# Performance work log

Measured on AMD Instinct MI355X. Metric: run time of the kernel, lower is better.

Reference implementation:

```python
import jax, jax.numpy as jnp
import numpy as np
from jax import lax

EPS = 1e-5
N_CROPS = 501
CROP_W = 500
RF = 65          # temporal receptive field
KS = 15          # conv1 kernel size
POOL = 3


def _bn(x, g, b, m, v, axis=1):
    shp = [1] * x.ndim
    shp[axis] = -1
    inv = g.reshape(shp) / jnp.sqrt(v.reshape(shp) + EPS)
    return (x - m.reshape(shp)) * inv + b.reshape(shp)


def setup_inputs() -> dict:
    key = jax.random.key(0)
    ks = jax.random.split(key, 16)
    B, C_IN, CH, T = 16, 1, 22, 1001
    F = 36
    OUT = 4
    FLAT = F * 43  # 1548 (corrected fc in_features; repo constant 504 is inconsistent)
    d = {
        "x": jax.random.normal(ks[0], (B, C_IN, CH, T), jnp.float32),
        # temporal conv [1,65]
        "w_t": jax.random.normal(ks[1], (F, 1, 1, RF), jnp.float32) * 0.1,
        "b_t": jax.random.normal(ks[2], (F,), jnp.float32) * 0.1,
        "bn_t_g": jax.random.uniform(ks[3], (F,), jnp.float32, 0.5, 1.5),
        "bn_t_b": jax.random.normal(ks[4], (F,), jnp.float32) * 0.1,
        "bn_t_m": jax.random.normal(ks[5], (F,), jnp.float32) * 0.1,
        "bn_t_v": jax.random.uniform(ks[6], (F,), jnp.float32, 0.5, 1.5),
        # spatial conv [22,1]
        "w_s": jax.random.normal(ks[7], (F, F, CH, 1), jnp.float32) * 0.05,
        "b_s": jax.random.normal(ks[8], (F,), jnp.float32) * 0.1,
        "bn_s_g": jax.random.uniform(ks[9], (F,), jnp.float32, 0.5, 1.5),
        "bn_s_b": jax.random.normal(ks[10], (F,), jnp.float32) * 0.1,
        "bn_s_m": jax.random.normal(ks[11], (F,), jnp.float32) * 0.1,
        "bn_s_v": jax.random.uniform(ks[12], (F,), jnp.float32, 0.5, 1.5),
        # conv1 [1,15] (as 1-D conv over time)
        "w_c": jax.random.normal(ks[13], (F, F, KS), jnp.float32) * 0.05,
        "b_c": jax.random.normal(ks[14], (F,), jnp.float32) * 0.1,
        "bn_c_g": jnp.ones((F,), jnp.float32),
        "bn_c_b": jnp.zeros((F,), jnp.float32),
        "bn_c_m": jnp.zeros((F,), jnp.float32),
        "bn_c_v": jnp.ones((F,), jnp.float32),
        # fc
        "w_fc": jax.random.normal(ks[15], (OUT, FLAT), jnp.float32) * 0.02,
        "b_fc": jnp.zeros((OUT,), jnp.float32),
    }
    return d


def reference(x, w_t, b_t, bn_t_g, bn_t_b, bn_t_m, bn_t_v,
              w_s, b_s, bn_s_g, bn_s_b, bn_s_m, bn_s_v,
              w_c, b_c, bn_c_g, bn_c_b, bn_c_m, bn_c_v,
              w_fc, b_fc):
    B = x.shape[0]
    F = w_t.shape[0]
    OUT = b_fc.shape[0]

    # temporal + spatial conv/BN/ELU are shift-invariant -> compute once over full T
    h = lax.conv_general_dilated(x, w_t, (1, 1), 'VALID',
                                 dimension_numbers=('NCHW', 'OIHW', 'NCHW'))
    h = h + b_t[None, :, None, None]                       # [B,36,22,937]
    h = jax.nn.elu(_bn(h, bn_t_g, bn_t_b, bn_t_m, bn_t_v))
    h = lax.conv_general_dilated(h, w_s, (1, 1), 'VALID',
                                 dimension_numbers=('NCHW', 'OIHW', 'NCHW'))
    h = h + b_s[None, :, None, None]                       # [B,36,1,937]
    h = jax.nn.elu(_bn(h, bn_s_g, bn_s_b, bn_s_m, bn_s_v))
    h = h[:, :, 0, :]                                      # [B,36,937]

    TW = CROP_W - RF + 1  # 436: temporal width of each crop after temporal conv

    def crop_logits(i):
        sl = lax.dynamic_slice_in_dim(h, i, TW, axis=2)    # [B,36,436]
        p1 = sl[:, :, :435].reshape(B, F, 145, POOL).mean(-1)  # avgpool1 -> [B,36,145]
        c = lax.conv_general_dilated(p1, w_c, (1,), 'VALID',
                                     dimension_numbers=('NCH', 'OIH', 'NCH'))
        c = c + b_c[None, :, None]                          # [B,36,131]
        c = jax.nn.elu(_bn(c, bn_c_g, bn_c_b, bn_c_m, bn_c_v))
        p2 = c[:, :, :129].reshape(B, F, 43, POOL).mean(-1)  # avgpool2 -> [B,36,43]
        flat = p2.reshape(B, -1)                            # [B,1548]
        return flat @ w_fc.T + b_fc                         # [B,OUT]

    def step(acc, i):
        return acc + crop_logits(i), None

    init = jnp.zeros((B, OUT), x.dtype)
    total, _ = lax.scan(step, init, jnp.arange(N_CROPS))
    return total / N_CROPS
```

## Files before the change

### kernel.cpp

```cpp
#include <hip/hip_runtime.h>

#define EPS 1e-5f
#define B 16
#define CH 22
#define CH2 24
#define T_IN 1001
#define F 36
#define RF 65
#define T1 937
#define FC 792
#define UN 885
#define PSP 944
#define KS 15
#define GN 295
#define WN 129
#define M43 43
#define BF 576
#define FLAT 1548

#define H2_OFF  0
#define A_OFF   539712
#define P_OFF   1049472
#define WTT_OFF 4617792
#define WST_OFF 4620132
#define WCQ_OFF 4651236
#define BN_OFF  4677156

__device__ __forceinline__ float elu_f(float v) {
    return v > 0.f ? v : (__expf(v) - 1.f);
}

__global__ __launch_bounds__(256) void k_prep(
    const float* __restrict__ w_t, const float* __restrict__ w_s,
    const float* __restrict__ w_c,
    const float* __restrict__ b_t, const float* __restrict__ g_t,
    const float* __restrict__ be_t,const float* __restrict__ m_t,
    const float* __restrict__ v_t,
    const float* __restrict__ b_s, const float* __restrict__ g_s,
    const float* __restrict__ be_s,const float* __restrict__ m_s,
    const float* __restrict__ v_s,
    const float* __restrict__ b_c, const float* __restrict__ g_c,
    const float* __restrict__ be_c,const float* __restrict__ m_c,
    const float* __restrict__ v_c, const float* __restrict__ b_fc,
    float* __restrict__ wtT, float* __restrict__ wsTp,
    float* __restrict__ wcQ, float* __restrict__ bnz,
    float* __restrict__ out)
{
    int i = blockIdx.x * 256 + threadIdx.x;
    if (i < F * RF)     { int k = i / F,  fi = i % F; wtT[i] = w_t[fi * RF + k]; }
    if (i < F * CH2 * F) {
        int fi = i / (CH2 * F);
        int r  = i % (CH2 * F);
        int ch = r / F, fo = r % F;
        wsTp[i] = (ch < CH) ? w_s[(fo * F + fi) * CH + ch] : 0.f;
    }
    if (i < 12 * 36 * 15 * 4) {
        int t3 = i / (36 * 15 * 4);
        int r  = i % (36 * 15 * 4);
        int f  = r / 60;
        int r2 = r % 60;
        int k  = r2 / 4, j = r2 % 4;
        wcQ[i] = (j < 3) ? w_c[((3 * t3 + j) * F + f) * KS + k] : 0.f;
    }
    if (i < F) {
        float s1 = g_t[i] * rsqrtf(v_t[i] + EPS);
        bnz[i]          = s1;
        bnz[F + i]      = (b_t[i] - m_t[i]) * s1 + be_t[i];
        float s2 = g_s[i] * rsqrtf(v_s[i] + EPS);
        bnz[2 * F + i]  = s2;
        bnz[3 * F + i]  = (b_s[i] - m_s[i]) * s2 + be_s[i];
        float s3 = g_c[i] * rsqrtf(v_c[i] + EPS);
        bnz[4 * F + i]  = s3;
        bnz[5 * F + i]  = (b_c[i] - m_c[i]) * s3 + be_c[i];
    }
    if (i < B * 4) out[i] = b_fc[i & 3];
}

__global__ __launch_bounds__(1024, 4) void k_fused(
    const float* __restrict__ x, const float* __restrict__ wtT,
    const float* __restrict__ wsTp, const float* __restrict__ bnz,
    float* __restrict__ h2)
{
    __shared__ float xs[CH2 * 128];
    __shared__ float comb[8][64][F];
    const int tid  = threadIdx.x;
    const int lane = tid & 63;
    const int w = __builtin_amdgcn_readfirstlane(tid >> 6);
    const int q = w >> 2;
    const int g = w & 3;
    const int b  = blockIdx.y;
    const int t0 = blockIdx.x * 64;

    for (int i = tid; i < CH2 * 128; i += 1024) {
        int ch = i >> 7, j = i & 127;
        int t = t0 + j; if (t > T_IN - 1) t = T_IN - 1;
        xs[i] = (ch < CH) ? x[(b * CH + ch) * T_IN + t] : 0.f;
    }
    __syncthreads();

    const int ch0 = q * 6;
    const int fi0 = g * 9;

    float acc[F];
    #pragma unroll
    for (int fo = 0; fo < F; ++fo) acc[fo] = 0.f;

    for (int c = 0; c < 6; ++c) {
        const float* xr = xs + (ch0 + c) * 128 + lane;

        float h1a[9];
        #pragma unroll
        for (int j = 0; j < 9; ++j) h1a[j] = 0.f;

        #pragma unroll 8
        for (int kp = 0; kp < 32; ++kp) {
            const int k = 2 * kp;
            float xv0 = xr[k];
            float xv1 = xr[k + 1];
            const float* w0 = wtT + k * F + fi0;
            const float* w1 = w0 + F;
            #pragma unroll
            for (int j = 0; j < 9; ++j) {
                h1a[j] += xv0 * w0[j];
                h1a[j] += xv1 * w1[j];
            }
        }
        {
            float xv = xr[64];
            const float* w64 = wtT + 64 * F + fi0;
            #pragma unroll
            for (int j = 0; j < 9; ++j) h1a[j] += xv * w64[j];
        }

        #pragma unroll
        for (int j = 0; j < 9; ++j)
            h1a[j] = elu_f(h1a[j] * bnz[fi0 + j] + bnz[F + fi0 + j]);

        #pragma unroll
        for (int j = 0; j < 9; ++j) {
            const float* wr = wsTp + ((fi0 + j) * CH2 + ch0 + c) * F;
            float e = h1a[j];
            #pragma unroll
            for (int fo = 0; fo < F; ++fo)
                acc[fo] += e * wr[fo];
        }
    }

    for (int half = 8; half >= 1; half >>= 1) {
        if (w >= half && w < 2 * half) {
            float4* cb = (float4*)&comb[w - half][lane][0];
            #pragma unroll
            for (int j = 0; j < 9; ++j)
                cb[j] = make_float4(acc[4*j], acc[4*j+1], acc[4*j+2], acc[4*j+3]);
        }
        __syncthreads();
        if (w < half) {
            const float4* cb = (const float4*)&comb[w][lane][0];
            #pragma unroll
            for (int j = 0; j < 9; ++j) {
                float4 v = cb[j];
                acc[4*j]   += v.x; acc[4*j+1] += v.y;
                acc[4*j+2] += v.z; acc[4*j+3] += v.w;
            }
        }
        __syncthreads();
    }

    if (w == 0) {
        int t = t0 + lane;
        if (t < T1) {
            #pragma unroll
            for (int fo = 0; fo < F; ++fo) {
                float s2 = bnz[2 * F + fo], o2 = bnz[3 * F + fo];
                h2[(b * F + fo) * T1 + t] = elu_f(acc[fo] * s2 + o2);
            }
        }
    }
}

__global__ __launch_bounds__(256) void k_pool(
    const float* __restrict__ h2, float* __restrict__ P)
{
    const int bf = blockIdx.x;
    const float* hr = h2 + (size_t)bf * T1;
    float* Pr = P + (size_t)bf * PSP;
    for (int i = threadIdx.x; i < PSP; i += 256) {
        int s0 = i     < T1 - 1 ? i     : T1 - 1;
        int s1 = i + 1 < T1 - 1 ? i + 1 : T1 - 1;
        int s2 = i + 2 < T1 - 1 ? i + 2 : T1 - 1;
        Pr[i] = (hr[s0] + hr[s1] + hr[s2]) * (1.f / 3.f);
    }
}

__global__ __launch_bounds__(768) void k_qconv(
    const float* __restrict__ P, const float* __restrict__ wcQ,
    const float* __restrict__ bnz, float* __restrict__ A)
{
    const int tid  = threadIdx.x;
    const int lane = tid & 63;
    const int t3 = __builtin_amdgcn_readfirstlane(tid >> 6);
    const int b  = blockIdx.y;
    const int u0 = blockIdx.x * 64;
    const int fo0 = t3 * 3;

    const float* wq = wcQ + t3 * (36 * 60);

    float a0 = 0.f, a1 = 0.f, a2 = 0.f;

    for (int f = 0; f < F; ++f) {
        const float* Pr = P + (size_t)(b * F + f) * PSP + u0 + lane;
        const float* wf = wq + f * 60;
        #pragma unroll
        for (int k = 0; k < KS; ++k) {
            float pv = Pr[3 * k];
            a0 += pv * wf[4 * k + 0];
            a1 += pv * wf[4 * k + 1];
            a2 += pv * wf[4 * k + 2];
        }
    }

    int u = u0 + lane;
    if (u < UN) {
        float sc0 = bnz[4 * F + fo0 + 0], oc0 = bnz[5 * F + fo0 + 0];
        float sc1 = bnz[4 * F + fo0 + 1], oc1 = bnz[5 * F + fo0 + 1];
        float sc2 = bnz[4 * F + fo0 + 2], oc2 = bnz[5 * F + fo0 + 2];
        A[((size_t)(b * F + fo0 + 0)) * UN + u] = elu_f(a0 * sc0 + oc0);
        A[((size_t)(b * F + fo0 + 1)) * UN + u] = elu_f(a1 * sc1 + oc1);
        A[((size_t)(b * F + fo0 + 2)) * UN + u] = elu_f(a2 * sc2 + oc2);
    }
}

__global__ __launch_bounds__(256) void k_wins(
    const float* __restrict__ A, const float* __restrict__ w_fc,
    float* __restrict__ out)
{
    __shared__ float Es[UN];
    __shared__ float G[GN];
    __shared__ float Ws[WN];
    __shared__ float Sm[M43];
    const int tid = threadIdx.x;
    const int bf = blockIdx.x;
    const int b = bf / F, f = bf % F;
    for (int i = tid; i < UN; i += 256)
        Es[i] = A[(size_t)bf * UN + i];
    __syncthreads();
    for (int q = tid; q < GN; q += 256)
        G[q] = Es[3 * q] + Es[3 * q + 1] + Es[3 * q + 2];
    __syncthreads();
    if (tid < WN) {
        float a = 0.f;
        for (int q = tid; q < tid + 167; ++q) a += G[q];
        Ws[tid] = a;
    }
    __syncthreads();
    if (tid < M43)
        Sm[tid] = (Ws[3 * tid] + Ws[3 * tid + 1] + Ws[3 * tid + 2]) * (1.f / 3.f);
    __syncthreads();
    if (tid < 4) {
        const float* wr = w_fc + tid * FLAT + f * M43;
        float a = 0.f;
        #pragma unroll 43
        for (int m = 0; m < M43; ++m) a += Sm[m] * wr[m];
        atomicAdd(&out[b * 4 + tid], a * (1.f / 501.f));
    }
}

extern "C" void kernel_launch(void* const* d_in, const int* in_sizes, int n_in,
                              void* d_out, int out_size, void* d_ws, size_t ws_size,
                              hipStream_t stream) {
    const float* x    = (const float*)d_in[0];
    const float* w_t  = (const float*)d_in[1];
    const float* b_t  = (const float*)d_in[2];
    const float* g_t  = (const float*)d_in[3];
    const float* be_t = (const float*)d_in[4];
    const float* m_t  = (const float*)d_in[5];
    const float* v_t  = (const float*)d_in[6];
    const float* w_s  = (const float*)d_in[7];
    const float* b_s  = (const float*)d_in[8];
    const float* g_s  = (const float*)d_in[9];
    const float* be_s = (const float*)d_in[10];
    const float* m_s  = (const float*)d_in[11];
    const float* v_s  = (const float*)d_in[12];
    const float* w_c  = (const float*)d_in[13];
    const float* b_c  = (const float*)d_in[14];
    const float* g_c  = (const float*)d_in[15];
    const float* be_c = (const float*)d_in[16];
    const float* m_c  = (const float*)d_in[17];
    const float* v_c  = (const float*)d_in[18];
    const float* w_fc = (const float*)d_in[19];
    const float* b_fc = (const float*)d_in[20];

    float* ws   = (float*)d_ws;
    float* h2   = ws + H2_OFF;
    float* A    = ws + A_OFF;
    float* P    = ws + P_OFF;
    float* wtT  = ws + WTT_OFF;
    float* wsTp = ws + WST_OFF;
    float* wcQ  = ws + WCQ_OFF;
    float* bnz  = ws + BN_OFF;
    float* out  = (float*)d_out;

    k_prep<<<dim3(128), 256, 0, stream>>>(
        w_t, w_s, w_c, b_t, g_t, be_t, m_t, v_t,
        b_s, g_s, be_s, m_s, v_s, b_c, g_c, be_c, m_c, v_c, b_fc,
        wtT, wsTp, wcQ, bnz, out);

    k_fused<<<dim3(15, B), 1024, 0, stream>>>(x, wtT, wsTp, bnz, h2);
    k_pool<<<dim3(BF), 256, 0, stream>>>(h2, P);
    k_qconv<<<dim3(14, B), 768, 0, stream>>>(P, wcQ, bnz, A);
    k_wins<<<dim3(BF), 256, 0, stream>>>(A, w_fc, out);
}
```

Before: 200.3 us.

## Split fused conv channel reduction across grid z and finish in pool kernel

The fused temporal+spatial conv kernel now launches 8 channel-group slices along grid z with 256-thread blocks instead of 1024-thread blocks handling all channels, writing partial sums to a new buffer. The pool kernel sums the 8 partials, applies BN+ELU, and stages the row in shared memory before average pooling. This raises block count and occupancy and shortens the in-block LDS reduction tree. In exchange it adds roughly 8x more intermediate global traffic for the partial buffer and an extra reduction pass.

```diff
diff --git a/kernel.cpp b/kernel.cpp
--- a/kernel.cpp
+++ b/kernel.cpp
@@ -8,7 +8,6 @@
 #define F 36
 #define RF 65
 #define T1 937
-#define FC 792
 #define UN 885
 #define PSP 944
 #define KS 15
@@ -17,14 +16,15 @@
 #define M43 43
 #define BF 576
 #define FLAT 1548
-
-#define H2_OFF  0
-#define A_OFF   539712
-#define P_OFF   1049472
-#define WTT_OFF 4617792
-#define WST_OFF 4620132
-#define WCQ_OFF 4651236
-#define BN_OFF  4677156
+#define NZ 8
+
+#define P_OFF   0
+#define A_OFF   543744
+#define H2P_OFF 1053504
+#define WTT_OFF 5366880
+#define WST_OFF 5369220
+#define WCQ_OFF 5400324
+#define BN_OFF  5426244
 
 __device__ __forceinline__ float elu_f(float v) {
     return v > 0.f ? v : (__expf(v) - 1.f);
@@ -76,37 +76,36 @@
     if (i < B * 4) out[i] = b_fc[i & 3];
 }
 
-__global__ __launch_bounds__(1024, 4) void k_fused(
+__global__ __launch_bounds__(256) void k_fused(
     const float* __restrict__ x, const float* __restrict__ wtT,
     const float* __restrict__ wsTp, const float* __restrict__ bnz,
-    float* __restrict__ h2)
-{
-    __shared__ float xs[CH2 * 128];
-    __shared__ float comb[8][64][F];
+    float* __restrict__ h2p)
+{
+    __shared__ float xs[3 * 128];
+    __shared__ float comb[2][64][F];
     const int tid  = threadIdx.x;
     const int lane = tid & 63;
     const int w = __builtin_amdgcn_readfirstlane(tid >> 6);
-    const int q = w >> 2;
-    const int g = w & 3;
     const int b  = blockIdx.y;
+    const int z  = blockIdx.z;
     const int t0 = blockIdx.x * 64;
-
-    for (int i = tid; i < CH2 * 128; i += 1024) {
-        int ch = i >> 7, j = i & 127;
+    const int ch0 = z * 3;
+    const int fi0 = w * 9;
+
+    for (int i = tid; i < 3 * 128; i += 256) {
+        int c = i >> 7, j = i & 127;
+        int ch = ch0 + c;
         int t = t0 + j; if (t > T_IN - 1) t = T_IN - 1;
         xs[i] = (ch < CH) ? x[(b * CH + ch) * T_IN + t] : 0.f;
     }
     __syncthreads();
-
-    const int ch0 = q * 6;
-    const int fi0 = g * 9;
 
     float acc[F];
     #pragma unroll
     for (int fo = 0; fo < F; ++fo) acc[fo] = 0.f;
 
-    for (int c = 0; c < 6; ++c) {
-        const float* xr = xs + (ch0 + c) * 128 + lane;
+    for (int c = 0; c < 3; ++c) {
+        const float* xr = xs + c * 128 + lane;
 
         float h1a[9];
         #pragma unroll
@@ -146,49 +145,69 @@
         }
     }
 
-    for (int half = 8; half >= 1; half >>= 1) {
-        if (w >= half && w < 2 * half) {
-            float4* cb = (float4*)&comb[w - half][lane][0];
-            #pragma unroll
-            for (int j = 0; j < 9; ++j)
-                cb[j] = make_float4(acc[4*j], acc[4*j+1], acc[4*j+2], acc[4*j+3]);
-        }
-        __syncthreads();
-        if (w < half) {
-            const float4* cb = (const float4*)&comb[w][lane][0];
-            #pragma unroll
-            for (int j = 0; j < 9; ++j) {
-                float4 v = cb[j];
-                acc[4*j]   += v.x; acc[4*j+1] += v.y;
-                acc[4*j+2] += v.z; acc[4*j+3] += v.w;
-            }
-        }
-        __syncthreads();
-    }
-
+    if (w >= 2) {
+        float4* cb = (float4*)&comb[w - 2][lane][0];
+        #pragma unroll
+        for (int j = 0; j < 9; ++j)
+            cb[j] = make_float4(acc[4*j], acc[4*j+1], acc[4*j+2], acc[4*j+3]);
+    }
+    __syncthreads();
+    if (w < 2) {
+        const float4* cb = (const float4*)&comb[w][lane][0];
+        #pragma unroll
+        for (int j = 0; j < 9; ++j) {
+            float4 v = cb[j];
+            acc[4*j]   += v.x; acc[4*j+1] += v.y;
+            acc[4*j+2] += v.z; acc[4*j+3] += v.w;
+        }
+    }
+    __syncthreads();
+    if (w == 1) {
+        float4* cb = (float4*)&comb[0][lane][0];
+        #pragma unroll
+        for (int j = 0; j < 9; ++j)
+            cb[j] = make_float4(acc[4*j], acc[4*j+1], acc[4*j+2], acc[4*j+3]);
+    }
+    __syncthreads();
     if (w == 0) {
+        const float4* cb = (const float4*)&comb[0][lane][0];
+        #pragma unroll
+        for (int j = 0; j < 9; ++j) {
+            float4 v = cb[j];
+            acc[4*j]   += v.x; acc[4*j+1] += v.y;
+            acc[4*j+2] += v.z; acc[4*j+3] += v.w;
+        }
         int t = t0 + lane;
         if (t < T1) {
             #pragma unroll
-            for (int fo = 0; fo < F; ++fo) {
-                float s2 = bnz[2 * F + fo], o2 = bnz[3 * F + fo];
-                h2[(b * F + fo) * T1 + t] = elu_f(acc[fo] * s2 + o2);
-            }
-        }
-    }
-}
-
-__global__ __launch_bounds__(256) void k_pool(
-    const float* __restrict__ h2, float* __restrict__ P)
-{
+            for (int fo = 0; fo < F; ++fo)
+                h2p[((size_t)(z * BF + b * F + fo)) * T1 + t] = acc[fo];
+        }
+    }
+}
+
+__global__ __launch_bounds__(256) void k_hpool(
+    const float* __restrict__ h2p, const float* __restrict__ bnz,
+    float* __restrict__ P)
+{
+    __shared__ float Ls[T1];
     const int bf = blockIdx.x;
-    const float* hr = h2 + (size_t)bf * T1;
+    const int f = bf % F;
+    const float s2 = bnz[2 * F + f], o2 = bnz[3 * F + f];
+    for (int i = threadIdx.x; i < T1; i += 256) {
+        float s = 0.f;
+        #pragma unroll
+        for (int z = 0; z < NZ; ++z)
+            s += h2p[((size_t)(z * BF + bf)) * T1 + i];
+        Ls[i] = elu_f(s * s2 + o2);
+    }
+    __syncthreads();
     float* Pr = P + (size_t)bf * PSP;
     for (int i = threadIdx.x; i < PSP; i += 256) {
         int s0 = i     < T1 - 1 ? i     : T1 - 1;
         int s1 = i + 1 < T1 - 1 ? i + 1 : T1 - 1;
-        int s2 = i + 2 < T1 - 1 ? i + 2 : T1 - 1;
-        Pr[i] = (hr[s0] + hr[s1] + hr[s2]) * (1.f / 3.f);
+        int s2i= i + 2 < T1 - 1 ? i + 2 : T1 - 1;
+        Pr[i] = (Ls[s0] + Ls[s1] + Ls[s2i]) * (1.f / 3.f);
     }
 }
 
@@ -291,9 +310,9 @@
     const float* b_fc = (const float*)d_in[20];
 
     float* ws   = (float*)d_ws;
-    float* h2   = ws + H2_OFF;
+    float* P    = ws + P_OFF;
     float* A    = ws + A_OFF;
-    float* P    = ws + P_OFF;
+    float* h2p  = ws + H2P_OFF;
     float* wtT  = ws + WTT_OFF;
     float* wsTp = ws + WST_OFF;
     float* wcQ  = ws + WCQ_OFF;
@@ -305,8 +324,8 @@
         b_s, g_s, be_s, m_s, v_s, b_c, g_c, be_c, m_c, v_c, b_fc,
         wtT, wsTp, wcQ, bnz, out);
 
-    k_fused<<<dim3(15, B), 1024, 0, stream>>>(x, wtT, wsTp, bnz, h2);
-    k_pool<<<dim3(BF), 256, 0, stream>>>(h2, P);
+    k_fused<<<dim3(15, B, NZ), 256, 0, stream>>>(x, wtT, wsTp, bnz, h2p);
+    k_hpool<<<dim3(BF), 256, 0, stream>>>(h2p, bnz, P);
     k_qconv<<<dim3(14, B), 768, 0, stream>>>(P, wcQ, bnz, A);
     k_wins<<<dim3(BF), 256, 0, stream>>>(A, w_fc, out);
 }
```

Result: no change. 201.6 us (+0.6%).
